# Performance work log

Hardware: AMD Instinct MI355X
Metric: run time of the kernel (lower is better)

Reference implementation:

```python
import jax, jax.numpy as jnp
import numpy as np

B, L, D = 4, 2048, 1024
N, K, H = 8, 1, 128
FG, FA = 4096, 2048
SEP = 1792
SOFTCAP = 50.0
EPS = 1e-6
BIG_NEG = -2.3819763e38


def setup_inputs() -> dict:
    key = jax.random.key(0)
    ks = jax.random.split(key, 16)
    def rnd(k, shape, s=0.02):
        return jax.random.normal(k, shape, dtype=jnp.float32) * s
    return {
        "x": rnd(ks[0], (B, L, D), 1.0),
        "positions": jnp.broadcast_to(jnp.arange(L + 1, dtype=jnp.int32), (B, L + 1)),
        "attn_mask": jnp.ones((B, 1, L, L), dtype=bool),
        "separation_idx": SEP,
        "pre_attn_scale": rnd(ks[1], (D,), 0.1),
        "pre_ffw_scale": rnd(ks[2], (D,), 0.1),
        "g_qw": rnd(ks[3], (N, D, H)),
        "g_kvw": rnd(ks[4], (2, K, D, H)),
        "g_ow": rnd(ks[5], (N, H, D)),
        "a_qw": rnd(ks[6], (N, D, H)),
        "a_kvw": rnd(ks[7], (2, K, D, H)),
        "a_ow": rnd(ks[8], (N, H, D)),
        "g_gate": rnd(ks[9], (2, D, FG)),
        "g_lin": rnd(ks[10], (FG, D)),
        "a_gate": rnd(ks[11], (2, D, FA)),
        "a_lin": rnd(ks[12], (FA, D)),
    }


def rms_norm(x, scale):
    var = jnp.mean(jnp.square(x), axis=-1, keepdims=True)
    return x * jax.lax.rsqrt(var + EPS) * (1.0 + scale)


def apply_rope(x, positions, max_wavelength=10_000.0):
    # x: [B,T,n,H], positions: [B,T]
    hd = x.shape[-1]
    frac = 2.0 * jnp.arange(hd // 2, dtype=jnp.float32) / hd
    timescale = max_wavelength ** frac  # [H/2]
    radians = positions.astype(jnp.float32)[:, :, None, None] / timescale  # [B,T,1,H/2]
    sin, cos = jnp.sin(radians), jnp.cos(radians)
    x1, x2 = jnp.split(x, 2, axis=-1)
    return jnp.concatenate([x1 * cos - x2 * sin, x2 * cos + x1 * sin], axis=-1).astype(x.dtype)


def get_qkv(xn, pos, qw, kvw):
    q = jnp.einsum('btd,ndh->btnh', xn, qw)
    q = apply_rope(q, pos) * (H ** -0.5)  # query_pre_attn_norm == 'rsqrt_head_dim'
    k = apply_rope(jnp.einsum('btd,kdh->btkh', xn, kvw[0]), pos)
    v = jnp.einsum('btd,kdh->btkh', xn, kvw[1])
    return q, k, v


def attention(q, k, v, mask):
    b, t, n, h = q.shape
    kk = k.shape[2]
    g = n // kk
    qg = q.reshape(b, t, kk, g, h)
    logits = jnp.einsum('btkgh,bskh->bkgts', qg, k)
    logits = SOFTCAP * jnp.tanh(logits / SOFTCAP)
    logits = jnp.where(mask[:, :, None], logits, BIG_NEG)  # mask [B,1,T,S] -> [B,1,1,T,S]
    probs = jax.nn.softmax(logits.astype(jnp.float32), axis=-1).astype(q.dtype)
    return jnp.einsum('bkgts,bskh->btkgh', probs, v).reshape(b, t, n, h)


def ffn(x, gate, lin):
    h = jax.nn.gelu(jnp.einsum('btd,df->btf', x, gate[0])) * jnp.einsum('btd,df->btf', x, gate[1])
    return jnp.einsum('btf,fd->btd', h, lin)


def process(attn_out, residual, ffw_scale, gate, lin):
    # post_norms=False, dropout=0: out = mlp(norm(attn + res)) + res (per source)
    h = rms_norm(attn_out + residual, ffw_scale)
    return ffn(h, gate, lin) + residual


def reference(x, positions, attn_mask, separation_idx, pre_attn_scale, pre_ffw_scale,
              g_qw, g_kvw, g_ow, a_qw, a_kvw, a_ow, g_gate, g_lin, a_gate, a_lin):
    sep = separation_idx
    x_g, x_a = x[:, :sep], x[:, sep:]
    n_g = rms_norm(x_g, pre_attn_scale)
    n_a = rms_norm(x_a, pre_attn_scale)
    p_g = positions[:, :sep]
    p_a = positions[:, sep + 1:]
    qg, kg, vg = get_qkv(n_g, p_g, g_qw, g_kvw)
    qa, ka, va = get_qkv(n_a, p_a, a_qw, a_kvw)
    q = jnp.concatenate([qg, qa], axis=1)
    k = jnp.concatenate([kg, ka], axis=1)
    v = jnp.concatenate([vg, va], axis=1)
    attn = attention(q, k, v, attn_mask)  # [B,L,N,H]
    go = jnp.einsum('btnh,nhd->btd', attn[:, :sep], g_ow)
    ao = jnp.einsum('btnh,nhd->btd', attn[:, sep:], a_ow)
    out_g = process(go, x_g, pre_ffw_scale, g_gate, g_lin)
    out_a = process(ao, x_a, pre_ffw_scale, a_gate, a_lin)
    return jnp.concatenate([out_g, out_a], axis=1)
```

## Files before the change

kernel.cpp:

```cpp
#include <hip/hip_runtime.h>
#include <hip/hip_bf16.h>
#include <stdint.h>

typedef short s8b __attribute__((ext_vector_type(8)));
typedef float f4 __attribute__((ext_vector_type(4)));
typedef unsigned short u16t;
typedef unsigned int u32t;

#define AS1 __attribute__((address_space(1)))
#define AS3 __attribute__((address_space(3)))
#define DEVFN static __device__ __forceinline__

DEVFN u16t f2b(float f){ union{ __hip_bfloat16 h; u16t u; } c; c.h = __float2bfloat16(f); return c.u; }

DEVFN float geluf(float x){
  float t = 0.7978845608028654f*(x + 0.044715f*x*x*x);
  t = fminf(fmaxf(t, -15.0f), 15.0f);
  float e = __expf(2.0f*t);
  return 0.5f*x*(1.0f + (e-1.0f)/(e+1.0f));
}
DEVFN float softcapf(float x){
  float t = x*0.02f;
  t = fminf(fmaxf(t, -15.0f), 15.0f);
  float e = __expf(2.0f*t);
  return 50.0f*(e-1.0f)/(e+1.0f);
}

__global__ void pack_qkv_k(u16t* dst, const float* qw, const float* kvw){
  int i = blockIdx.x*256 + threadIdx.x;
  if(i >= 1280*1024) return;
  int row = i >> 10, d = i & 1023;
  float v;
  if(row < 1024){ int n = row >> 7, h = row & 127; v = qw[(n*1024 + d)*128 + h]; }
  else if(row < 1152){ v = kvw[d*128 + (row-1024)]; }
  else { v = kvw[131072 + d*128 + (row-1152)]; }
  dst[i] = f2b(v);
}
__global__ void pack_ot_k(u16t* dst, const float* ow){
  int i = blockIdx.x*256 + threadIdx.x;
  if(i >= 1024*1024) return;
  int dd = i >> 10, nh = i & 1023;
  dst[i] = f2b(ow[nh*1024 + dd]);
}
__global__ void pack_gate_k(u16t* dst, const float* gate, int F, int total){
  int i = blockIdx.x*256 + threadIdx.x;
  if(i >= total) return;
  int r = i >> 10, dd = i & 1023;
  dst[i] = f2b(gate[(r&1)*(1024*F) + dd*F + (r>>1)]);
}
__global__ void pack_lin_k(u16t* dst, const float* lin, int lf, int total){
  int i = blockIdx.x*256 + threadIdx.x;
  if(i >= total) return;
  int dd = i >> lf, f = i & ((1<<lf)-1);
  dst[i] = f2b(lin[f*1024 + dd]);
}

__global__ __launch_bounds__(256) void rmsnorm_k(const float* __restrict__ x, const float* __restrict__ sc,
                                                 u16t* __restrict__ out){
  int row = blockIdx.x;
  int tid = threadIdx.x;
  const float* xr = x + (size_t)row*1024;
  float4 v = *(const float4*)(xr + tid*4);
  float s = v.x*v.x + v.y*v.y + v.z*v.z + v.w*v.w;
  #pragma unroll
  for(int off=32; off>=1; off>>=1) s += __shfl_down(s, off);
  __shared__ float ws4[4];
  if((tid & 63) == 0) ws4[tid>>6] = s;
  __syncthreads();
  float tot = ws4[0]+ws4[1]+ws4[2]+ws4[3];
  float r = rsqrtf(tot*(1.0f/1024.0f) + 1e-6f);
  float4 scv = *(const float4*)(sc + tid*4);
  u16t o0 = f2b(v.x*r*(1.0f+scv.x)), o1 = f2b(v.y*r*(1.0f+scv.y));
  u16t o2 = f2b(v.z*r*(1.0f+scv.z)), o3 = f2b(v.w*r*(1.0f+scv.w));
  uint2 pk; pk.x = (u32t)o0 | ((u32t)o1<<16); pk.y = (u32t)o2 | ((u32t)o3<<16);
  *(uint2*)(out + (size_t)row*1024 + tid*4) = pk;
}

__global__ __launch_bounds__(256) void rope_k(const float* __restrict__ qkv, u16t* __restrict__ qb,
                                              u16t* __restrict__ kswz, u16t* __restrict__ vrow){
  int row = blockIdx.x;
  int b = row >> 11, t = row & 2047;
  float pos = (float)(t + (t >= 1792 ? 1 : 0));
  const float* src = qkv + (size_t)row*1280;
  size_t kvbase = ((size_t)b*2048 + t)*128;
  int swz = ((t&7)<<3) ^ (((t>>3)&3)<<4);
  for(int idx = threadIdx.x; idx < 704; idx += 256){
    if(idx < 512){
      int n = idx >> 6, i = idx & 63;
      float inv = exp2f((float)i * -0.20762050593046f);
      float sn, cs; sincosf(pos*inv, &sn, &cs);
      float x1 = src[n*128+i], x2 = src[n*128+i+64];
      const float qs = 0.08838834764831845f;
      qb[(size_t)row*1024 + n*128 + i]      = f2b((x1*cs - x2*sn)*qs);
      qb[(size_t)row*1024 + n*128 + i + 64] = f2b((x2*cs + x1*sn)*qs);
    } else if(idx < 576){
      int i = idx - 512;
      float inv = exp2f((float)i * -0.20762050593046f);
      float sn, cs; sincosf(pos*inv, &sn, &cs);
      float x1 = src[1024+i], x2 = src[1024+i+64];
      kswz[kvbase + (i ^ swz)]        = f2b(x1*cs - x2*sn);
      kswz[kvbase + ((i+64) ^ swz)]   = f2b(x2*cs + x1*sn);
    } else {
      int h = idx - 576;
      vrow[kvbase + h] = f2b(src[1152+h]);
    }
  }
}

__global__ __launch_bounds__(256) void vt_pack_k(const u16t* __restrict__ vrow, u16t* __restrict__ vtswz){
  int blk = blockIdx.x;
  int b = blk >> 5, kt = blk & 31;
  int tid = threadIdx.x;
  const u16t* src = vrow + ((size_t)b*2048 + kt*64)*128;
  #pragma unroll
  for(int it=0; it<4; ++it){
    int o = it*2048 + tid*8;
    int d = o >> 6, kg = o & 63;
    u16t tmp[8];
    #pragma unroll
    for(int j=0;j<8;j++) tmp[j] = src[(size_t)(kg+j)*128 + d];
    *(uint4*)&vtswz[((size_t)b*128 + d)*2048 + kt*64 + (kg ^ ((d&7)<<3))] = *(const uint4*)tmp;
  }
}

struct GemmArgs {
  const u16t* A; int lda;
  const u16t* Bg; const u16t* Ba;
  int K; int ntN; int mode; int amap; int omap; int ep;
  float* outf; u16t* outb; int ldo;
  const float* res;
};

__global__ __launch_bounds__(256) void gemm_k(GemmArgs g){
  __shared__ __align__(16) u16t As[2*128*32];
  __shared__ __align__(16) u16t Bs[2*128*32];
  int bid = blockIdx.x;
  int mt = bid / g.ntN, nt = bid % g.ntN;
  int c0 = mt*128, g0;
  const u16t* B;
  if(g.mode == 0){
    g0 = c0;
    B = ((mt & 15) < 14) ? g.Bg : g.Ba;
  } else if(g.mode == 1){
    int bb = mt/14, t = (mt - bb*14)*128;
    g0 = bb*2048 + t; B = g.Bg;
  } else {
    int bb = mt>>1, t = 1792 + (mt&1)*128;
    g0 = bb*2048 + t; B = g.Bg;
  }
  int arow = g.amap ? g0 : c0;
  int orow = g.omap ? g0 : c0;
  int tid = threadIdx.x, lane = tid & 63, w = tid >> 6, l15 = lane & 15, lg = lane >> 4;
  int wr = w >> 1, wc = w & 1;

  const u16t* Ap = g.A + (size_t)(arow + (tid>>2))*g.lda + (tid&3)*8;
  const u16t* Bp = B   + (size_t)(nt*128 + (tid>>2))*g.K + (tid&3)*8;
  size_t lda64 = (size_t)64*g.lda, ldb64 = (size_t)64*g.K;
  u32t le = tid*8;

  f4 acc[4][4];
  #pragma unroll
  for(int mi=0;mi<4;mi++)
    #pragma unroll
    for(int ni=0;ni<4;ni++){ f4 z = {0.0f,0.0f,0.0f,0.0f}; acc[mi][ni]=z; }

  auto stagef = [&](int buf, int k0){
    u16t* a = As + buf*4096;
    u16t* b = Bs + buf*4096;
    __builtin_amdgcn_global_load_lds((const AS1 u32t*)(Ap + k0),          (AS3 u32t*)&a[le],        16,0,0);
    __builtin_amdgcn_global_load_lds((const AS1 u32t*)(Ap + k0 + lda64),  (AS3 u32t*)&a[le + 2048], 16,0,0);
    __builtin_amdgcn_global_load_lds((const AS1 u32t*)(Bp + k0),          (AS3 u32t*)&b[le],        16,0,0);
    __builtin_amdgcn_global_load_lds((const AS1 u32t*)(Bp + k0 + ldb64),  (AS3 u32t*)&b[le + 2048], 16,0,0);
  };

  stagef(0, 0);
  __syncthreads();
  int cur = 0;
  for(int k0=0; k0 < g.K; k0 += 32){
    if(k0 + 32 < g.K) stagef(cur^1, k0+32);
    const u16t* as = As + cur*4096;
    const u16t* bs = Bs + cur*4096;
    s8b af[4], bf[4];
    #pragma unroll
    for(int mi=0;mi<4;mi++) af[mi] = *(const s8b*)&as[(wr*64 + mi*16 + l15)*32 + lg*8];
    #pragma unroll
    for(int ni=0;ni<4;ni++) bf[ni] = *(const s8b*)&bs[(wc*64 + ni*16 + l15)*32 + lg*8];
    #pragma unroll
    for(int mi=0;mi<4;mi++)
      #pragma unroll
      for(int ni=0;ni<4;ni++)
        acc[mi][ni] = __builtin_amdgcn_mfma_f32_16x16x32_bf16(af[mi], bf[ni], acc[mi][ni], 0,0,0);
    __syncthreads();
    cur ^= 1;
  }

  #pragma unroll
  for(int mi=0;mi<4;mi++){
    #pragma unroll
    for(int ni=0;ni<4;ni++){
      int rowb = wr*64 + mi*16 + lg*4;
      int col = nt*128 + wc*64 + ni*16 + l15;
      #pragma unroll
      for(int r=0;r<4;r++){
        float v = acc[mi][ni][r];
        size_t ro = (size_t)(orow + rowb + r);
        if(g.ep == 0){
          g.outf[ro*(size_t)g.ldo + col] = v;
        } else if(g.ep == 1){
          g.outf[ro*(size_t)g.ldo + col] = v + g.res[ro*1024 + col];
        } else {
          float other = __shfl_xor(v, 1);
          if((lane & 1) == 0){
            g.outb[ro*(size_t)g.ldo + (col>>1)] = f2b(geluf(v)*other);
          }
        }
      }
    }
  }
}

__global__ __launch_bounds__(256) void attn_k(const u16t* __restrict__ qb, const u16t* __restrict__ kswz,
                                              const u16t* __restrict__ vtswz, u16t* __restrict__ attnb){
  __shared__ __align__(16) u16t Ks[64*128];
  __shared__ __align__(16) u16t Vt[128*64];
  __shared__ __align__(16) u16t Ps[4*16*72];
  int bid = blockIdx.x;
  int qt = bid & 31, n = (bid>>5)&7, b = bid>>8;
  int tid = threadIdx.x, lane = tid&63, w = tid>>6, l15 = lane&15, lg = lane>>4;
  int q0 = qt*64 + w*16;

  s8b qf[4];
  const u16t* qrow = qb + ((size_t)(b*2048 + q0 + l15)*8 + n)*128;
  #pragma unroll
  for(int kc=0;kc<4;kc++) qf[kc] = *(const s8b*)(qrow + kc*32 + lg*8);

  float lsum[4];
  f4 oacc[8];
  #pragma unroll
  for(int r=0;r<4;r++) lsum[r] = 0.0f;
  #pragma unroll
  for(int db=0;db<8;db++){ f4 z = {0.0f,0.0f,0.0f,0.0f}; oacc[db]=z; }

  const u16t* kbase  = kswz  + (size_t)b*2048*128;
  const u16t* vtbase = vtswz + (size_t)b*128*2048;
  u16t* psw = Ps + w*1152;

  for(int st=0; st<32; ++st){
    const u16t* kt  = kbase  + (size_t)st*64*128;
    const u16t* vtb = vtbase + st*64;
    __syncthreads();
    #pragma unroll
    for(int it=0; it<4; ++it){
      int e = it*2048 + tid*8;
      __builtin_amdgcn_global_load_lds((const AS1 u32t*)(kt + e), (AS3 u32t*)&Ks[e], 16,0,0);
    }
    #pragma unroll
    for(int it=0; it<4; ++it){
      int e = it*2048 + tid*8;
      int d = e >> 6, ko = e & 63;
      __builtin_amdgcn_global_load_lds((const AS1 u32t*)(vtb + (size_t)d*2048 + ko), (AS3 u32t*)&Vt[e], 16,0,0);
    }
    __syncthreads();

    f4 sf[4];
    #pragma unroll
    for(int kb=0;kb<4;kb++){ f4 z = {0.0f,0.0f,0.0f,0.0f}; sf[kb]=z; }
    #pragma unroll
    for(int kb=0;kb<4;kb++){
      int key = kb*16 + l15;
      int swz = ((key&7)<<3) ^ (((key>>3)&3)<<4);
      #pragma unroll
      for(int kc=0;kc<4;kc++){
        s8b kf = *(const s8b*)&Ks[key*128 + ((kc*32 + lg*8) ^ swz)];
        sf[kb] = __builtin_amdgcn_mfma_f32_16x16x32_bf16(qf[kc], kf, sf[kb], 0,0,0);
      }
    }
    #pragma unroll
    for(int r=0;r<4;r++){
      int prow = lg*4 + r;
      #pragma unroll
      for(int kb=0;kb<4;kb++){
        float pv = __expf(softcapf(sf[kb][r]));
        lsum[r] += pv;
        psw[prow*72 + kb*16 + l15] = f2b(pv);
      }
    }
    #pragma unroll
    for(int kc2=0;kc2<2;kc2++){
      s8b pa = *(const s8b*)&psw[l15*72 + kc2*32 + lg*8];
      int koff = (kc2*32 + lg*8) ^ ((l15&7)<<3);
      #pragma unroll
      for(int db=0;db<8;db++){
        s8b vf = *(const s8b*)&Vt[(db*16 + l15)*64 + koff];
        oacc[db] = __builtin_amdgcn_mfma_f32_16x16x32_bf16(pa, vf, oacc[db], 0,0,0);
      }
    }
  }

  float linv[4];
  #pragma unroll
  for(int r=0;r<4;r++){
    float s = lsum[r];
    #pragma unroll
    for(int off=1; off<16; off<<=1) s += __shfl_xor(s, off);
    linv[r] = 1.0f / s;
  }

  #pragma unroll
  for(int db=0;db<8;db++){
    #pragma unroll
    for(int r=0;r<4;r++){
      int qrowi = q0 + lg*4 + r;
      int d = db*16 + l15;
      attnb[(size_t)(b*2048 + qrowi)*1024 + n*128 + d] = f2b(oacc[db][r] * linv[r]);
    }
  }
}

extern "C" void kernel_launch(void* const* d_in, const int* in_sizes, int n_in,
                              void* d_out, int out_size, void* d_ws, size_t ws_size,
                              hipStream_t stream){
  const float* x        = (const float*)d_in[0];
  const float* pre_attn = (const float*)d_in[4];
  const float* pre_ffw  = (const float*)d_in[5];
  const float* g_qw  = (const float*)d_in[6];
  const float* g_kvw = (const float*)d_in[7];
  const float* g_ow  = (const float*)d_in[8];
  const float* a_qw  = (const float*)d_in[9];
  const float* a_kvw = (const float*)d_in[10];
  const float* a_ow  = (const float*)d_in[11];
  const float* g_gate= (const float*)d_in[12];
  const float* g_lin = (const float*)d_in[13];
  const float* a_gate= (const float*)d_in[14];
  const float* a_lin = (const float*)d_in[15];
  float* out = (float*)d_out;
  (void)in_sizes; (void)n_in; (void)out_size; (void)ws_size;

  char* wsp = (char*)d_ws; size_t off = 0;
  auto alloc = [&](size_t b){ void* p = wsp + off; off += (b + 255) & ~(size_t)255; return p; };
  u16t* wqkv_g = (u16t*)alloc((size_t)1280*1024*2);
  u16t* wqkv_a = (u16t*)alloc((size_t)1280*1024*2);
  u16t* wo_g   = (u16t*)alloc((size_t)1024*1024*2);
  u16t* wo_a   = (u16t*)alloc((size_t)1024*1024*2);
  u16t* wg_g   = (u16t*)alloc((size_t)8192*1024*2);
  u16t* wg_a   = (u16t*)alloc((size_t)4096*1024*2);
  u16t* wl_g   = (u16t*)alloc((size_t)1024*4096*2);
  u16t* wl_a   = (u16t*)alloc((size_t)1024*2048*2);
  u16t* xn     = (u16t*)alloc((size_t)8192*1024*2);
  u16t* xn2    = xn;
  char* big    = (char*)alloc((size_t)7168*4096*2);
  float* qkv   = (float*)big;
  float* t1    = (float*)big;
  u16t* hid_g  = (u16t*)big;
  u16t* qb     = (u16t*)alloc((size_t)8192*1024*2);
  u16t* kswz   = (u16t*)alloc((size_t)4*2048*128*2);
  u16t* vrow   = (u16t*)alloc((size_t)4*2048*128*2);
  u16t* vtswz  = (u16t*)alloc((size_t)4*128*2048*2);
  u16t* attnb  = (u16t*)alloc((size_t)8192*1024*2);
  u16t* hid_a  = (u16t*)alloc((size_t)1024*2048*2);

  pack_qkv_k<<<(1280*1024+255)/256,256,0,stream>>>(wqkv_g, g_qw, g_kvw);
  pack_qkv_k<<<(1280*1024+255)/256,256,0,stream>>>(wqkv_a, a_qw, a_kvw);
  pack_ot_k <<<(1024*1024+255)/256,256,0,stream>>>(wo_g, g_ow);
  pack_ot_k <<<(1024*1024+255)/256,256,0,stream>>>(wo_a, a_ow);
  pack_gate_k<<<(8192*1024+255)/256,256,0,stream>>>(wg_g, g_gate, 4096, 8192*1024);
  pack_gate_k<<<(4096*1024+255)/256,256,0,stream>>>(wg_a, a_gate, 2048, 4096*1024);
  pack_lin_k<<<(1024*4096+255)/256,256,0,stream>>>(wl_g, g_lin, 12, 1024*4096);
  pack_lin_k<<<(1024*2048+255)/256,256,0,stream>>>(wl_a, a_lin, 11, 1024*2048);
  rmsnorm_k<<<8192,256,0,stream>>>(x, pre_attn, xn);

  { GemmArgs ga = {xn, 1024, wqkv_g, wqkv_a, 1024, 10, 0,0,0, 0, qkv, nullptr, 1280, nullptr};
    gemm_k<<<64*10,256,0,stream>>>(ga); }
  rope_k<<<8192,256,0,stream>>>(qkv, qb, kswz, vrow);
  vt_pack_k<<<128,256,0,stream>>>(vrow, vtswz);
  attn_k<<<1024,256,0,stream>>>(qb, kswz, vtswz, attnb);
  { GemmArgs ga = {attnb, 1024, wo_g, wo_a, 1024, 8, 0,0,0, 1, t1, nullptr, 1024, x};
    gemm_k<<<64*8,256,0,stream>>>(ga); }
  rmsnorm_k<<<8192,256,0,stream>>>(t1, pre_ffw, xn2);
  { GemmArgs ga = {xn2, 1024, wg_g, nullptr, 1024, 64, 1,1,0, 3, nullptr, hid_g, 4096, nullptr};
    gemm_k<<<56*64,256,0,stream>>>(ga); }
  { GemmArgs ga = {xn2, 1024, wg_a, nullptr, 1024, 32, 2,1,0, 3, nullptr, hid_a, 2048, nullptr};
    gemm_k<<<8*32,256,0,stream>>>(ga); }
  { GemmArgs ga = {hid_g, 4096, wl_g, nullptr, 4096, 8, 1,0,1, 1, out, nullptr, 1024, x};
    gemm_k<<<56*8,256,0,stream>>>(ga); }
  { GemmArgs ga = {hid_a, 2048, wl_a, nullptr, 2048, 8, 2,0,1, 1, out, nullptr, 1024, x};
    gemm_k<<<8*8,256,0,stream>>>(ga); }
}
```

Before: 955.1 us.

## Tile weight transposes through LDS and swizzle GEMM LDS layout

Replaces the per-element strided weight pack kernels with a single 32x32 LDS-tiled transpose kernel, so both the fp32 reads and the bf16 writes are coalesced. It also XOR-swizzles the 16-byte chunk positions in the GEMM's global-to-LDS staging and in the matching fragment reads, to cut LDS bank conflicts. More kernel launches are issued for the packing, and the swizzle has to stay consistent between the writer and reader sides.

```diff
diff --git a/kernel.cpp b/kernel.cpp
--- a/kernel.cpp
+++ b/kernel.cpp
@@ -26,33 +26,24 @@
   return 50.0f*(e-1.0f)/(e+1.0f);
 }
 
-__global__ void pack_qkv_k(u16t* dst, const float* qw, const float* kvw){
-  int i = blockIdx.x*256 + threadIdx.x;
-  if(i >= 1280*1024) return;
-  int row = i >> 10, d = i & 1023;
-  float v;
-  if(row < 1024){ int n = row >> 7, h = row & 127; v = qw[(n*1024 + d)*128 + h]; }
-  else if(row < 1152){ v = kvw[d*128 + (row-1024)]; }
-  else { v = kvw[131072 + d*128 + (row-1152)]; }
-  dst[i] = f2b(v);
-}
-__global__ void pack_ot_k(u16t* dst, const float* ow){
-  int i = blockIdx.x*256 + threadIdx.x;
-  if(i >= 1024*1024) return;
-  int dd = i >> 10, nh = i & 1023;
-  dst[i] = f2b(ow[nh*1024 + dd]);
-}
-__global__ void pack_gate_k(u16t* dst, const float* gate, int F, int total){
-  int i = blockIdx.x*256 + threadIdx.x;
-  if(i >= total) return;
-  int r = i >> 10, dd = i & 1023;
-  dst[i] = f2b(gate[(r&1)*(1024*F) + dd*F + (r>>1)]);
-}
-__global__ void pack_lin_k(u16t* dst, const float* lin, int lf, int total){
-  int i = blockIdx.x*256 + threadIdx.x;
-  if(i >= total) return;
-  int dd = i >> lf, f = i & ((1<<lf)-1);
-  dst[i] = f2b(lin[f*1024 + dd]);
+__global__ __launch_bounds__(256) void tpack_k(u16t* __restrict__ dst, const float* __restrict__ src,
+                                               int ldsrc, int lddst, int rmul, int roff, int prow,
+                                               size_t pstride){
+  __shared__ float tile[32][33];
+  int z = blockIdx.z;
+  const float* s = src + (size_t)z*pstride;
+  int f0 = blockIdx.x*32, d0 = blockIdx.y*32;
+  int t = threadIdx.x, r = t>>5, c = t&31;
+  #pragma unroll
+  for(int i=0;i<4;i++)
+    tile[r + i*8][c] = s[(size_t)(d0 + r + i*8)*ldsrc + f0 + c];
+  __syncthreads();
+  int rbase = roff + z*prow;
+  #pragma unroll
+  for(int i=0;i<4;i++){
+    int f = f0 + r + i*8;
+    dst[(size_t)(f*rmul + rbase)*lddst + d0 + c] = f2b(tile[c][r + i*8]);
+  }
 }
 
 __global__ __launch_bounds__(256) void rmsnorm_k(const float* __restrict__ x, const float* __restrict__ sc,
@@ -153,10 +144,18 @@
   int tid = threadIdx.x, lane = tid & 63, w = tid >> 6, l15 = lane & 15, lg = lane >> 4;
   int wr = w >> 1, wc = w & 1;
 
-  const u16t* Ap = g.A + (size_t)(arow + (tid>>2))*g.lda + (tid&3)*8;
-  const u16t* Bp = B   + (size_t)(nt*128 + (tid>>2))*g.K + (tid&3)*8;
+  int gsrc = ((tid&3) ^ ((tid>>3)&3))*8;
+  const u16t* Ap = g.A + (size_t)(arow + (tid>>2))*g.lda + gsrc;
+  const u16t* Bp = B   + (size_t)(nt*128 + (tid>>2))*g.K + gsrc;
   size_t lda64 = (size_t)64*g.lda, ldb64 = (size_t)64*g.K;
   u32t le = tid*8;
+
+  int xr = (lg ^ ((l15>>1)&3))*8;
+  int aoff[4], boff[4];
+  #pragma unroll
+  for(int mi=0;mi<4;mi++) aoff[mi] = (wr*64 + mi*16 + l15)*32 + xr;
+  #pragma unroll
+  for(int ni=0;ni<4;ni++) boff[ni] = (wc*64 + ni*16 + l15)*32 + xr;
 
   f4 acc[4][4];
   #pragma unroll
@@ -182,9 +181,9 @@
     const u16t* bs = Bs + cur*4096;
     s8b af[4], bf[4];
     #pragma unroll
-    for(int mi=0;mi<4;mi++) af[mi] = *(const s8b*)&as[(wr*64 + mi*16 + l15)*32 + lg*8];
-    #pragma unroll
-    for(int ni=0;ni<4;ni++) bf[ni] = *(const s8b*)&bs[(wc*64 + ni*16 + l15)*32 + lg*8];
+    for(int mi=0;mi<4;mi++) af[mi] = *(const s8b*)&as[aoff[mi]];
+    #pragma unroll
+    for(int ni=0;ni<4;ni++) bf[ni] = *(const s8b*)&bs[boff[ni]];
     #pragma unroll
     for(int mi=0;mi<4;mi++)
       #pragma unroll
@@ -359,14 +358,19 @@
   u16t* attnb  = (u16t*)alloc((size_t)8192*1024*2);
   u16t* hid_a  = (u16t*)alloc((size_t)1024*2048*2);
 
-  pack_qkv_k<<<(1280*1024+255)/256,256,0,stream>>>(wqkv_g, g_qw, g_kvw);
-  pack_qkv_k<<<(1280*1024+255)/256,256,0,stream>>>(wqkv_a, a_qw, a_kvw);
-  pack_ot_k <<<(1024*1024+255)/256,256,0,stream>>>(wo_g, g_ow);
-  pack_ot_k <<<(1024*1024+255)/256,256,0,stream>>>(wo_a, a_ow);
-  pack_gate_k<<<(8192*1024+255)/256,256,0,stream>>>(wg_g, g_gate, 4096, 8192*1024);
-  pack_gate_k<<<(4096*1024+255)/256,256,0,stream>>>(wg_a, a_gate, 2048, 4096*1024);
-  pack_lin_k<<<(1024*4096+255)/256,256,0,stream>>>(wl_g, g_lin, 12, 1024*4096);
-  pack_lin_k<<<(1024*2048+255)/256,256,0,stream>>>(wl_a, a_lin, 11, 1024*2048);
+  tpack_k<<<dim3(4,32,8),256,0,stream>>>(wqkv_g, g_qw, 128, 1024, 1, 0, 128, 131072);
+  tpack_k<<<dim3(4,32,1),256,0,stream>>>(wqkv_g, g_kvw, 128, 1024, 1, 1024, 0, 0);
+  tpack_k<<<dim3(4,32,1),256,0,stream>>>(wqkv_g, g_kvw + 131072, 128, 1024, 1, 1152, 0, 0);
+  tpack_k<<<dim3(4,32,8),256,0,stream>>>(wqkv_a, a_qw, 128, 1024, 1, 0, 128, 131072);
+  tpack_k<<<dim3(4,32,1),256,0,stream>>>(wqkv_a, a_kvw, 128, 1024, 1, 1024, 0, 0);
+  tpack_k<<<dim3(4,32,1),256,0,stream>>>(wqkv_a, a_kvw + 131072, 128, 1024, 1, 1152, 0, 0);
+  tpack_k<<<dim3(32,32,1),256,0,stream>>>(wo_g, g_ow, 1024, 1024, 1, 0, 0, 0);
+  tpack_k<<<dim3(32,32,1),256,0,stream>>>(wo_a, a_ow, 1024, 1024, 1, 0, 0, 0);
+  tpack_k<<<dim3(128,32,2),256,0,stream>>>(wg_g, g_gate, 4096, 1024, 2, 0, 1, (size_t)1024*4096);
+  tpack_k<<<dim3(64,32,2),256,0,stream>>>(wg_a, a_gate, 2048, 1024, 2, 0, 1, (size_t)1024*2048);
+  tpack_k<<<dim3(32,128,1),256,0,stream>>>(wl_g, g_lin, 1024, 4096, 1, 0, 0, 0);
+  tpack_k<<<dim3(32,64,1),256,0,stream>>>(wl_a, a_lin, 1024, 2048, 1, 0, 0, 0);
+
   rmsnorm_k<<<8192,256,0,stream>>>(x, pre_attn, xn);
 
   { GemmArgs ga = {xn, 1024, wqkv_g, wqkv_a, 1024, 10, 0,0,0, 0, qkv, nullptr, 1280, nullptr};
```

Result: faster. 875.3 us (-8.4%).
